# Kernel optimization log

Hardware: AMD Instinct MI355X
Metric: run time of the kernel (lower is better)

Reference implementation:

```python
import jax, jax.numpy as jnp
import numpy as np

DEGREE = 8


def setup_inputs() -> dict:
    key = jax.random.key(0)
    k1, k2 = jax.random.split(key)
    b, c_in, c_out = 16384, 512, 512
    x = jax.random.normal(k1, (b, c_in), dtype=jnp.float32)
    std = 1.0 / (c_in * (DEGREE + 1))
    cheby_coeffs = jax.random.normal(k2, (c_in, c_out, DEGREE + 1), dtype=jnp.float32) * std
    return {"x": x, "cheby_coeffs": cheby_coeffs}


def reference(x, cheby_coeffs):
    # x: (b, c_in); cheby_coeffs: (c_in, c_out, degree+1)
    arange = jnp.arange(DEGREE + 1, dtype=x.dtype)  # (d+1,)
    # double tanh squashes into (-1, 1), then Chebyshev basis via acos/cos
    t = jnp.arccos(jnp.tanh(jnp.tanh(x)))            # (b, c_in)
    basis = jnp.cos(t[:, :, None] * arange)          # (b, c_in, d+1)
    y = jnp.einsum('bid,iod->bo', basis, cheby_coeffs)
    return y
```

## Files before the change

### kernel.cpp

```cpp
#include <hip/hip_runtime.h>
#include <hip/hip_bf16.h>
#include <stdint.h>

#define CIN   512
#define COUT  512
#define BM    128
#define BN    256
#define NIB   16
#define KSTEPS 128

typedef float f32x4 __attribute__((ext_vector_type(4)));
typedef short s16x8 __attribute__((ext_vector_type(8)));

__device__ uint4 Wp_g[KSTEPS * 32 * 64];
__device__ float bias_g[COUT];

__device__ __forceinline__ uint32_t cvtpk(float lo, float hi) {
  uint32_t r;
  asm("v_cvt_pk_bf16_f32 %0, %1, %2" : "=v"(r) : "v"(lo), "v"(hi));
  return r;
}

__device__ __forceinline__ float ftanh(float v) {
  float e = __expf(v + v);
  return 1.0f - __fdividef(2.0f, e + 1.0f);
}

__global__ void pack_w(const float* __restrict__ cw) {
  __shared__ float lf[32 * 144];
  int ib = blockIdx.x >> 5;
  int cg = blockIdx.x & 31;
  for (int r = threadIdx.x; r < 32 * 144; r += 256) {
    int il = r / 144;
    int rem = r - il * 144;
    lf[r] = cw[(size_t)(ib * 32 + il) * (COUT * 9) + cg * 144 + rem];
  }
  __syncthreads();
  for (int v = threadIdx.x; v < 512; v += 256) {
    int ksl = v >> 6;
    int lane = v & 63;
    int d = ksl + 1;
    int lh = lane >> 4, l15 = lane & 15;
    uint32_t p[4];
    #pragma unroll
    for (int q = 0; q < 4; ++q) {
      float a = lf[(lh * 8 + 2 * q    ) * 144 + l15 * 9 + d];
      float b = lf[(lh * 8 + 2 * q + 1) * 144 + l15 * 9 + d];
      p[q] = cvtpk(a, b);
    }
    Wp_g[((ib * 8 + ksl) * 32 + cg) * 64 + lane] = make_uint4(p[0], p[1], p[2], p[3]);
  }
}

__global__ void bias_k(const float* __restrict__ cw) {
  int o = blockIdx.x;
  int t = threadIdx.x;
  float s = 0.f;
  #pragma unroll
  for (int q = 0; q < 8; ++q)
    s += cw[(size_t)(t + 64 * q) * (COUT * 9) + o * 9];
  #pragma unroll
  for (int off = 32; off; off >>= 1) s += __shfl_down(s, off);
  if (t == 0) bias_g[o] = s;
}

__global__ void __launch_bounds__(1024, 4) cheby_gemm(const float* __restrict__ x,
                                                      float* __restrict__ out) {
  __shared__ uint4 lds[2 * 4 * 4 * BM];
  const int tid  = threadIdx.x;
  const int lane = tid & 63;
  const int l15  = lane & 15;
  const int lh   = lane >> 4;
  const int w    = tid >> 6;
  const int wr   = w >> 3;
  const int wc   = w & 7;
  const bool genw = (w < 8);

  int b0  = blockIdx.x;
  int bid = (b0 & 7) * 32 + (b0 >> 3);
  const int rb  = (bid >> 1) * BM;
  const int cb  = bid & 1;
  const int ocb = cb * BN;
  const int cgbase = cb * 16 + wc * 2;

  const int ge   = (w & 7) >> 1;
  const int grow = (w & 1) * 64 + lane;
  const float* xrow = x + (size_t)(rb + grow) * CIN + ge * 8;

  const uint4* pB = Wp_g + (size_t)cgbase * 64 + lane;

  f32x4 acc[4][2];
  #pragma unroll
  for (int cf = 0; cf < 2; ++cf) {
    float bv = bias_g[ocb + wc * 32 + cf * 16 + l15];
    #pragma unroll
    for (int rf = 0; rf < 4; ++rf) {
      acc[rf][cf][0] = bv; acc[rf][cf][1] = bv;
      acc[rf][cf][2] = bv; acc[rf][cf][3] = bv;
    }
  }

  float xv[8], u2[8], tm1[8], tm2[8];

  auto loadX = [&](int ib) {
    const float4* p = reinterpret_cast<const float4*>(xrow + ib * 32);
    float4 v0 = p[0], v1 = p[1];
    xv[0] = v0.x; xv[1] = v0.y; xv[2] = v0.z; xv[3] = v0.w;
    xv[4] = v1.x; xv[5] = v1.y; xv[6] = v1.z; xv[7] = v1.w;
  };
  auto compute_u = [&]() {
    #pragma unroll
    for (int k = 0; k < 8; ++k) {
      float u = ftanh(ftanh(xv[k]));
      tm1[k] = u; tm2[k] = 1.0f; u2[k] = u + u;
    }
  };
  auto advance = [&]() {
    #pragma unroll
    for (int k = 0; k < 8; ++k) {
      float t = __builtin_fmaf(u2[k], tm1[k], -tm2[k]);
      tm2[k] = tm1[k]; tm1[k] = t;
    }
  };
  auto emit = [&](int buf, int slot) {
    uint32_t p0 = cvtpk(tm1[0], tm1[1]);
    uint32_t p1 = cvtpk(tm1[2], tm1[3]);
    uint32_t p2 = cvtpk(tm1[4], tm1[5]);
    uint32_t p3 = cvtpk(tm1[6], tm1[7]);
    lds[((buf * 4 + slot) * 4 + ge) * BM + grow] = make_uint4(p0, p1, p2, p3);
  };

  s16x8 breg[2][2];
  auto loadB = [&](int par, int ks) {
    #pragma unroll
    for (int cf = 0; cf < 2; ++cf) {
      uint4 v = pB[(size_t)ks * 2048 + cf * 64];
      breg[par][cf] = __builtin_bit_cast(s16x8, v);
    }
  };
  auto mfma_step = [&](int buf, int slot, int par) {
    s16x8 a[4];
    int base = ((buf * 4 + slot) * 4 + lh) * BM + wr * 64 + l15;
    #pragma unroll
    for (int rf = 0; rf < 4; ++rf)
      a[rf] = *reinterpret_cast<const s16x8*>(&lds[base + rf * 16]);
    __builtin_amdgcn_s_setprio(1);
    #pragma unroll
    for (int rf = 0; rf < 4; ++rf) {
      #pragma unroll
      for (int cf = 0; cf < 2; ++cf)
        acc[rf][cf] = __builtin_amdgcn_mfma_f32_16x16x32_bf16(
            a[rf], breg[par][cf], acc[rf][cf], 0, 0, 0);
    }
    __builtin_amdgcn_s_setprio(0);
  };

  if (genw) {
    loadX(0);
    compute_u();
    emit(0, 0);
    advance(); emit(0, 1);
    advance(); emit(0, 2);
    advance(); emit(0, 3);
  }
  loadB(0, 0);
  __syncthreads();

  for (int ib = 0; ib < NIB; ++ib) {
    if (genw && ib + 1 < NIB) loadX(ib + 1);

    #pragma unroll
    for (int j = 0; j < 4; ++j) {
      int ks = ib * 8 + j;
      loadB((j + 1) & 1, ks + 1);
      mfma_step(0, j, j & 1);
      if (genw) { advance(); emit(1, j); }
    }
    __syncthreads();

    #pragma unroll
    for (int j = 0; j < 4; ++j) {
      int ks = ib * 8 + 4 + j;
      if (ks + 1 < KSTEPS) loadB((j + 1) & 1, ks + 1);
      mfma_step(1, j, j & 1);
      if (genw && ib + 1 < NIB) {
        if (j == 0) { compute_u(); emit(0, 0); }
        else        { advance();   emit(0, j); }
      }
    }
    __syncthreads();
  }

  const int orow = rb + wr * 64 + lh * 4;
  const int ocol = ocb + wc * 32 + l15;
  #pragma unroll
  for (int rf = 0; rf < 4; ++rf) {
    #pragma unroll
    for (int cf = 0; cf < 2; ++cf) {
      #pragma unroll
      for (int r = 0; r < 4; ++r)
        out[(size_t)(orow + rf * 16 + r) * COUT + ocol + cf * 16] = acc[rf][cf][r];
    }
  }
}

extern "C" void kernel_launch(void* const* d_in, const int* in_sizes, int n_in,
                              void* d_out, int out_size, void* d_ws, size_t ws_size,
                              hipStream_t stream) {
  const float* x  = (const float*)d_in[0];
  const float* cw = (const float*)d_in[1];
  float* out = (float*)d_out;

  pack_w<<<dim3(512), dim3(256), 0, stream>>>(cw);
  bias_k<<<dim3(COUT), dim3(64), 0, stream>>>(cw);
  cheby_gemm<<<dim3(256), dim3(1024), 0, stream>>>(x, out);
}
```

Baseline: 94.40 us.

## Double-buffer full 8-degree basis blocks to halve per-block barriers

Result: no change. 95.07 us (+0.7%).

```diff
diff --git a/kernel.cpp b/kernel.cpp
--- a/kernel.cpp
+++ b/kernel.cpp
@@ -8,6 +8,7 @@
 #define BN    256
 #define NIB   16
 #define KSTEPS 128
+#define SLOTS 8
 
 typedef float f32x4 __attribute__((ext_vector_type(4)));
 typedef short s16x8 __attribute__((ext_vector_type(8)));
@@ -24,6 +25,12 @@
 __device__ __forceinline__ float ftanh(float v) {
   float e = __expf(v + v);
   return 1.0f - __fdividef(2.0f, e + 1.0f);
+}
+
+__device__ __forceinline__ void lds_barrier() {
+  asm volatile("s_waitcnt lgkmcnt(0)" ::: "memory");
+  __builtin_amdgcn_s_barrier();
+  asm volatile("" ::: "memory");
 }
 
 __global__ void pack_w(const float* __restrict__ cw) {
@@ -66,7 +73,7 @@
 
 __global__ void __launch_bounds__(1024, 4) cheby_gemm(const float* __restrict__ x,
                                                       float* __restrict__ out) {
-  __shared__ uint4 lds[2 * 4 * 4 * BM];
+  __shared__ uint4 lds[2 * SLOTS * 4 * BM];
   const int tid  = threadIdx.x;
   const int lane = tid & 63;
   const int l15  = lane & 15;
@@ -127,7 +134,7 @@
     uint32_t p1 = cvtpk(tm1[2], tm1[3]);
     uint32_t p2 = cvtpk(tm1[4], tm1[5]);
     uint32_t p3 = cvtpk(tm1[6], tm1[7]);
-    lds[((buf * 4 + slot) * 4 + ge) * BM + grow] = make_uint4(p0, p1, p2, p3);
+    lds[((buf * SLOTS + slot) * 4 + ge) * BM + grow] = make_uint4(p0, p1, p2, p3);
   };
 
   s16x8 breg[2][2];
@@ -140,7 +147,7 @@
   };
   auto mfma_step = [&](int buf, int slot, int par) {
     s16x8 a[4];
-    int base = ((buf * 4 + slot) * 4 + lh) * BM + wr * 64 + l15;
+    int base = ((buf * SLOTS + slot) * 4 + lh) * BM + wr * 64 + l15;
     #pragma unroll
     for (int rf = 0; rf < 4; ++rf)
       a[rf] = *reinterpret_cast<const s16x8*>(&lds[base + rf * 16]);
@@ -159,36 +166,27 @@
     loadX(0);
     compute_u();
     emit(0, 0);
-    advance(); emit(0, 1);
-    advance(); emit(0, 2);
-    advance(); emit(0, 3);
+    #pragma unroll
+    for (int s = 1; s < 8; ++s) { advance(); emit(0, s); }
   }
   loadB(0, 0);
-  __syncthreads();
+  lds_barrier();
 
   for (int ib = 0; ib < NIB; ++ib) {
+    const int cur = ib & 1, nxt = cur ^ 1;
     if (genw && ib + 1 < NIB) loadX(ib + 1);
 
     #pragma unroll
-    for (int j = 0; j < 4; ++j) {
+    for (int j = 0; j < 8; ++j) {
       int ks = ib * 8 + j;
-      loadB((j + 1) & 1, ks + 1);
-      mfma_step(0, j, j & 1);
-      if (genw) { advance(); emit(1, j); }
-    }
-    __syncthreads();
-
-    #pragma unroll
-    for (int j = 0; j < 4; ++j) {
-      int ks = ib * 8 + 4 + j;
       if (ks + 1 < KSTEPS) loadB((j + 1) & 1, ks + 1);
-      mfma_step(1, j, j & 1);
+      mfma_step(cur, j, j & 1);
       if (genw && ib + 1 < NIB) {
-        if (j == 0) { compute_u(); emit(0, 0); }
-        else        { advance();   emit(0, j); }
+        if (j == 0) { compute_u(); emit(nxt, 0); }
+        else        { advance();   emit(nxt, j); }
       }
     }
-    __syncthreads();
+    lds_barrier();
   }
 
   const int orow = rb + wr * 64 + lh * 4;
```

## Switch to 32x32x16 MFMA with 512-thread blocks and per-phase barriers

Applied to the files above, without the earlier changes.

New measurement: 118.3 us. 1.25x slower.

```diff
diff --git a/kernel.cpp b/kernel.cpp
--- a/kernel.cpp
+++ b/kernel.cpp
@@ -5,14 +5,14 @@
 #define CIN   512
 #define COUT  512
 #define BM    128
-#define BN    256
+#define BN    128
 #define NIB   16
 #define KSTEPS 128
 
-typedef float f32x4 __attribute__((ext_vector_type(4)));
+typedef float f32x16 __attribute__((ext_vector_type(16)));
 typedef short s16x8 __attribute__((ext_vector_type(8)));
 
-__device__ uint4 Wp_g[KSTEPS * 32 * 64];
+__device__ uint4 Wp_g[KSTEPS * 2 * 16 * 64];
 __device__ float bias_g[COUT];
 
 __device__ __forceinline__ uint32_t cvtpk(float lo, float hi) {
@@ -27,28 +27,31 @@
 }
 
 __global__ void pack_w(const float* __restrict__ cw) {
-  __shared__ float lf[32 * 144];
-  int ib = blockIdx.x >> 5;
-  int cg = blockIdx.x & 31;
-  for (int r = threadIdx.x; r < 32 * 144; r += 256) {
-    int il = r / 144;
-    int rem = r - il * 144;
-    lf[r] = cw[(size_t)(ib * 32 + il) * (COUT * 9) + cg * 144 + rem];
+  __shared__ float lf[32 * 288];
+  int ib = blockIdx.x >> 4;
+  int cg = blockIdx.x & 15;
+  for (int r = threadIdx.x; r < 32 * 288; r += 256) {
+    int il = r / 288;
+    int rem = r - il * 288;
+    lf[r] = cw[(size_t)(ib * 32 + il) * (COUT * 9) + cg * 288 + rem];
   }
   __syncthreads();
-  for (int v = threadIdx.x; v < 512; v += 256) {
-    int ksl = v >> 6;
+  for (int v = threadIdx.x; v < 1024; v += 256) {
     int lane = v & 63;
-    int d = ksl + 1;
-    int lh = lane >> 4, l15 = lane & 15;
+    int kh   = (v >> 6) & 1;
+    int dm1  = v >> 7;
+    int d    = dm1 + 1;
+    int i0   = kh * 16 + (lane >> 5) * 8;
+    int ol   = lane & 31;
     uint32_t p[4];
     #pragma unroll
     for (int q = 0; q < 4; ++q) {
-      float a = lf[(lh * 8 + 2 * q    ) * 144 + l15 * 9 + d];
-      float b = lf[(lh * 8 + 2 * q + 1) * 144 + l15 * 9 + d];
+      float a = lf[(i0 + 2 * q    ) * 288 + ol * 9 + d];
+      float b = lf[(i0 + 2 * q + 1) * 288 + ol * 9 + d];
       p[q] = cvtpk(a, b);
     }
-    Wp_g[((ib * 8 + ksl) * 32 + cg) * 64 + lane] = make_uint4(p[0], p[1], p[2], p[3]);
+    Wp_g[(((ib * 8 + dm1) * 2 + kh) * 16 + cg) * 64 + lane] =
+        make_uint4(p[0], p[1], p[2], p[3]);
   }
 }
 
@@ -64,40 +67,37 @@
   if (t == 0) bias_g[o] = s;
 }
 
-__global__ void __launch_bounds__(1024, 4) cheby_gemm(const float* __restrict__ x,
-                                                      float* __restrict__ out) {
+__global__ void __launch_bounds__(512, 4) cheby_gemm(const float* __restrict__ x,
+                                                     float* __restrict__ out) {
   __shared__ uint4 lds[2 * 4 * 4 * BM];
   const int tid  = threadIdx.x;
   const int lane = tid & 63;
-  const int l15  = lane & 15;
-  const int lh   = lane >> 4;
+  const int l31  = lane & 31;
+  const int lh5  = lane >> 5;
   const int w    = tid >> 6;
-  const int wr   = w >> 3;
-  const int wc   = w & 7;
-  const bool genw = (w < 8);
+  const int wr   = w >> 2;
+  const int wc   = w & 3;
 
   int b0  = blockIdx.x;
-  int bid = (b0 & 7) * 32 + (b0 >> 3);
-  const int rb  = (bid >> 1) * BM;
-  const int cb  = bid & 1;
-  const int ocb = cb * BN;
-  const int cgbase = cb * 16 + wc * 2;
-
-  const int ge   = (w & 7) >> 1;
+  int bid = (b0 & 7) * 64 + (b0 >> 3);
+  const int rb   = (bid >> 2) * BM;
+  const int cb   = bid & 3;
+  const int ocb  = cb * BN;
+  const int cg32 = cb * 4 + wc;
+
+  const int ge   = w >> 1;
   const int grow = (w & 1) * 64 + lane;
   const float* xrow = x + (size_t)(rb + grow) * CIN + ge * 8;
 
-  const uint4* pB = Wp_g + (size_t)cgbase * 64 + lane;
-
-  f32x4 acc[4][2];
-  #pragma unroll
-  for (int cf = 0; cf < 2; ++cf) {
-    float bv = bias_g[ocb + wc * 32 + cf * 16 + l15];
-    #pragma unroll
-    for (int rf = 0; rf < 4; ++rf) {
-      acc[rf][cf][0] = bv; acc[rf][cf][1] = bv;
-      acc[rf][cf][2] = bv; acc[rf][cf][3] = bv;
-    }
+  const uint4* pB = Wp_g + (size_t)cg32 * 64 + lane;
+
+  f32x16 acc[2];
+  {
+    float bv = bias_g[ocb + wc * 32 + l31];
+    #pragma unroll
+    for (int rf = 0; rf < 2; ++rf)
+      #pragma unroll
+      for (int r = 0; r < 16; ++r) acc[rf][r] = bv;
   }
 
   float xv[8], u2[8], tm1[8], tm2[8];
@@ -133,73 +133,74 @@
   s16x8 breg[2][2];
   auto loadB = [&](int par, int ks) {
     #pragma unroll
-    for (int cf = 0; cf < 2; ++cf) {
-      uint4 v = pB[(size_t)ks * 2048 + cf * 64];
-      breg[par][cf] = __builtin_bit_cast(s16x8, v);
-    }
-  };
-  auto mfma_step = [&](int buf, int slot, int par) {
-    s16x8 a[4];
-    int base = ((buf * 4 + slot) * 4 + lh) * BM + wr * 64 + l15;
-    #pragma unroll
-    for (int rf = 0; rf < 4; ++rf)
-      a[rf] = *reinterpret_cast<const s16x8*>(&lds[base + rf * 16]);
+    for (int kh = 0; kh < 2; ++kh) {
+      uint4 v = pB[(size_t)(ks * 2 + kh) * 1024];
+      breg[par][kh] = __builtin_bit_cast(s16x8, v);
+    }
+  };
+
+  auto phase_mfma = [&](int buf, int slot, int par) {
+    s16x8 a[2][2];
+    #pragma unroll
+    for (int rf = 0; rf < 2; ++rf)
+      #pragma unroll
+      for (int kh = 0; kh < 2; ++kh)
+        a[rf][kh] = *reinterpret_cast<const s16x8*>(
+            &lds[((buf * 4 + slot) * 4 + 2 * kh + lh5) * BM + wr * 64 + rf * 32 + l31]);
+    asm volatile("s_waitcnt lgkmcnt(0)" ::: "memory");
+    __builtin_amdgcn_sched_barrier(0);
+    __builtin_amdgcn_s_barrier();
     __builtin_amdgcn_s_setprio(1);
     #pragma unroll
-    for (int rf = 0; rf < 4; ++rf) {
+    for (int kh = 0; kh < 2; ++kh)
       #pragma unroll
-      for (int cf = 0; cf < 2; ++cf)
-        acc[rf][cf] = __builtin_amdgcn_mfma_f32_16x16x32_bf16(
-            a[rf], breg[par][cf], acc[rf][cf], 0, 0, 0);
-    }
+      for (int rf = 0; rf < 2; ++rf)
+        acc[rf] = __builtin_amdgcn_mfma_f32_32x32x16_bf16(
+            a[rf][kh], breg[par][kh], acc[rf], 0, 0, 0);
     __builtin_amdgcn_s_setprio(0);
-  };
-
-  if (genw) {
-    loadX(0);
-    compute_u();
-    emit(0, 0);
-    advance(); emit(0, 1);
-    advance(); emit(0, 2);
-    advance(); emit(0, 3);
-  }
+    __builtin_amdgcn_s_barrier();
+  };
+
+  loadX(0);
+  compute_u();
+  emit(0, 0);
+  advance(); emit(0, 1);
+  advance(); emit(0, 2);
+  advance(); emit(0, 3);
   loadB(0, 0);
-  __syncthreads();
+  asm volatile("s_waitcnt lgkmcnt(0)" ::: "memory");
+  __builtin_amdgcn_sched_barrier(0);
+  __builtin_amdgcn_s_barrier();
 
   for (int ib = 0; ib < NIB; ++ib) {
-    if (genw && ib + 1 < NIB) loadX(ib + 1);
-
     #pragma unroll
     for (int j = 0; j < 4; ++j) {
       int ks = ib * 8 + j;
       loadB((j + 1) & 1, ks + 1);
-      mfma_step(0, j, j & 1);
-      if (genw) { advance(); emit(1, j); }
-    }
-    __syncthreads();
-
+      if (j == 0 && ib + 1 < NIB) loadX(ib + 1);
+      advance(); emit(1, j);
+      phase_mfma(0, j, j & 1);
+    }
     #pragma unroll
     for (int j = 0; j < 4; ++j) {
       int ks = ib * 8 + 4 + j;
       if (ks + 1 < KSTEPS) loadB((j + 1) & 1, ks + 1);
-      mfma_step(1, j, j & 1);
-      if (genw && ib + 1 < NIB) {
+      if (ib + 1 < NIB) {
         if (j == 0) { compute_u(); emit(0, 0); }
         else        { advance();   emit(0, j); }
       }
-    }
-    __syncthreads();
-  }
-
-  const int orow = rb + wr * 64 + lh * 4;
-  const int ocol = ocb + wc * 32 + l15;
+      phase_mfma(1, j, j & 1);
+    }
+  }
+
+  const int ocol  = ocb + wc * 32 + l31;
+  const int rbase = rb + wr * 64 + 4 * lh5;
   #pragma unroll
-  for (int rf = 0; rf < 4; ++rf) {
-    #pragma unroll
-    for (int cf = 0; cf < 2; ++cf) {
-      #pragma unroll
-      for (int r = 0; r < 4; ++r)
-        out[(size_t)(orow + rf * 16 + r) * COUT + ocol + cf * 16] = acc[rf][cf][r];
+  for (int rf = 0; rf < 2; ++rf) {
+    #pragma unroll
+    for (int r = 0; r < 16; ++r) {
+      int row = rbase + rf * 32 + (r & 3) + 8 * (r >> 2);
+      out[(size_t)row * COUT + ocol] = acc[rf][r];
     }
   }
 }
@@ -211,7 +212,7 @@
   const float* cw = (const float*)d_in[1];
   float* out = (float*)d_out;
 
-  pack_w<<<dim3(512), dim3(256), 0, stream>>>(cw);
+  pack_w<<<dim3(256), dim3(256), 0, stream>>>(cw);
   bias_k<<<dim3(COUT), dim3(64), 0, stream>>>(cw);
-  cheby_gemm<<<dim3(256), dim3(1024), 0, stream>>>(x, out);
-}
+  cheby_gemm<<<dim3(512), dim3(512), 0, stream>>>(x, out);
+}
```
